# Kernel tuning notes

Measured on AMD Instinct MI355X. Metric: run time of the kernel, lower is better.

## Reference

```python
import jax, jax.numpy as jnp
import numpy as np

B, T, C = 16, 512, 1024
D, K, W = 4096, 128, 8


def _scatter_topk(a, k, use_values):
    """Top-k along last axis; return dense array with top-k values (or 1.0) scattered, zeros elsewhere."""
    shp = a.shape
    a2 = a.reshape(-1, shp[-1])
    vals, idx = jax.lax.top_k(a2, k)
    rows = jnp.arange(a2.shape[0])[:, None]
    src = vals if use_values else jnp.ones_like(vals)
    return jnp.zeros_like(a2).at[rows, idx].set(src).reshape(shp)


def _window_topk(x, k, window_size):
    # x: (B, T, D)
    b, t, d = x.shape
    stride = max(1, window_size // 2)
    if stride >= t:
        num_windows, pad, t_pad = 1, 0, t
    else:
        num_windows = (t - window_size) // stride + 1
        required = (num_windows - 1) * stride + window_size
        pad = max(0, required - t)
        t_pad = t + pad
    if pad > 0:
        x = jnp.pad(x, ((0, 0), (0, pad), (0, 0)))
    starts = jnp.arange(num_windows) * stride                      # (NW,)
    tidx = starts[:, None] + jnp.arange(window_size)               # (NW, W)
    x_windows = x[:, tidx, :]                                      # (B, NW, W, D)
    window_sums = x_windows.sum(axis=2)                            # (B, NW, D)
    mask_windows = _scatter_topk(window_sums, k, use_values=False)  # (B, NW, D)
    votes = (x_windows * mask_windows[:, :, None, :]).reshape(b, num_windows * window_size, d)
    feature_votes = jnp.zeros((b, t_pad, d), x.dtype).at[:, tidx.reshape(-1)].add(votes)
    mask_combined = _scatter_topk(feature_votes, k, use_values=False)  # (B, Tp, D)
    x_sparse = x * mask_combined
    return x_sparse[:, :t - 0, :] if pad > 0 else x_sparse


def setup_inputs() -> dict:
    key = jax.random.key(0)
    ks = jax.random.split(key, 4)
    x_ssl = jax.random.normal(ks[0], (B, T, C), jnp.float32)
    W_dec = jax.random.normal(ks[1], (C, D), jnp.float32)
    W_dec = W_dec / jnp.linalg.norm(W_dec, axis=0, keepdims=True)
    W_enc = W_dec.T                                                # tied init, as in module
    W1 = jax.random.normal(ks[2], (256, D), jnp.float32) * (1.0 / np.sqrt(D))
    W2 = jax.random.normal(ks[3], (2, 256), jnp.float32) * (1.0 / np.sqrt(256))
    return dict(
        x_ssl=x_ssl, W_enc=W_enc, b_enc=jnp.zeros((D,), jnp.float32),
        W_dec=W_dec, b_dec=jnp.zeros((C,), jnp.float32),
        ln_g=jnp.ones((D,), jnp.float32), ln_b=jnp.zeros((D,), jnp.float32),
        W1=W1, b1=jnp.zeros((256,), jnp.float32),
        W2=W2, b2=jnp.zeros((2,), jnp.float32),
    )


def reference(x_ssl, W_enc, b_enc, W_dec, b_dec, ln_g, ln_b, W1, b1, W2, b2):
    b, t, c = x_ssl.shape
    x_flat = x_ssl.reshape(b * t, c)
    # SAE encode with window top-k (window_size=8 > 1 path)
    pre = jnp.einsum('nc,dc->nd', x_flat - b_dec, W_enc) + b_enc
    post_relu = jax.nn.relu(pre).reshape(b, t, -1)                 # (B, T, D)
    encoded = _window_topk(post_relu, K, W)                        # (B, T, D)
    encoded_flat = encoded.reshape(b * t, -1)
    # SAE decode + reconstruction loss
    x_recon = jnp.einsum('nd,cd->nc', encoded_flat, W_dec) + b_dec
    sae_loss = jnp.mean((x_recon - x_flat) ** 2)
    # classifier on pooled sparse features (dropout is inference no-op)
    pooled = encoded.mean(axis=1)                                  # (B, D) == AdaptiveAvgPool1d(1)
    mu = pooled.mean(axis=-1, keepdims=True)
    var = pooled.var(axis=-1, keepdims=True)
    ln = (pooled - mu) / jnp.sqrt(var + 1e-5) * ln_g + ln_b
    h = jax.nn.relu(ln @ W1.T + b1)
    logits = h @ W2.T + b2
    log_probs = jax.nn.log_softmax(logits, axis=-1)
    return log_probs, sae_loss
```

## Files before the change

### kernel.cpp

```cpp
#include <hip/hip_runtime.h>

#define BB   16
#define TT   512
#define CC   1024
#define DD   4096
#define NN   (BB*TT)
#define NWIN 127
#define KTOP 128

typedef __attribute__((ext_vector_type(8))) unsigned short ushort8;
typedef _Float16 half8 __attribute__((ext_vector_type(8)));
typedef __attribute__((ext_vector_type(4))) float f32x4;

__device__ __forceinline__ unsigned short f2h(float f) {
    union { _Float16 h; unsigned short u; } c;
    c.h = (_Float16)f;
    return c.u;
}
__device__ __forceinline__ float h2f(unsigned short u) {
    union { unsigned short u; _Float16 h; } c;
    c.u = u;
    return (float)c.h;
}
__device__ __forceinline__ unsigned tokey(float f) {
    unsigned u = __float_as_uint(f);
    return (u & 0x80000000u) ? ~u : (u | 0x80000000u);
}
__device__ __forceinline__ void async_lds16(const void* g, void* l) {
    __builtin_amdgcn_global_load_lds((const __attribute__((address_space(1))) void*)g,
                                     (__attribute__((address_space(3))) void*)l, 16, 0, 0);
}

#define PH_SYNC() do { __builtin_amdgcn_sched_barrier(0); __builtin_amdgcn_s_barrier(); \
                       asm volatile("s_waitcnt lgkmcnt(0)" ::: "memory"); \
                       __builtin_amdgcn_sched_barrier(0); __builtin_amdgcn_s_setprio(1); } while (0)
#define PH_END()  do { __builtin_amdgcn_s_setprio(0); __builtin_amdgcn_sched_barrier(0); \
                       __builtin_amdgcn_s_barrier(); } while (0)

__device__ __forceinline__ unsigned wave_prefix_incl(unsigned v) {
    int lane = threadIdx.x & 63;
#pragma unroll
    for (int off = 1; off < 64; off <<= 1) {
        unsigned n = __shfl_up(v, off, 64);
        if (lane >= off) v += n;
    }
    return v;
}
__device__ __forceinline__ unsigned wave_suffix_incl(unsigned v) {
    int lane = threadIdx.x & 63;
#pragma unroll
    for (int off = 1; off < 64; off <<= 1) {
        unsigned n = __shfl_down(v, off, 64);
        if (lane + off < 64) v += n;
    }
    return v;
}

__device__ __forceinline__ unsigned select_top128(const unsigned* keys,
                                                  unsigned* hist, unsigned* shx) {
    const int tid = threadIdx.x, wid = tid >> 6, lane = tid & 63;
    const unsigned ZKEY = 0x80000000u;
    unsigned cpos = 0, cz = 0;
#pragma unroll
    for (int i = 0; i < 16; ++i) {
        cpos += (keys[i] > ZKEY);
        cz   += (keys[i] == ZKEY);
    }
    unsigned ppos = wave_prefix_incl(cpos);
    unsigned pz   = wave_prefix_incl(cz);
    if (lane == 63) { shx[wid] = ppos; shx[4 + wid] = pz; }
    __syncthreads();
    unsigned nz = shx[0] + shx[1] + shx[2] + shx[3];
    unsigned selbits = 0u;
    if (nz <= KTOP) {
        unsigned need = KTOP - nz;
        unsigned zr = pz - cz;
        if (wid > 0) zr += shx[4];
        if (wid > 1) zr += shx[5];
        if (wid > 2) zr += shx[6];
#pragma unroll
        for (int i = 0; i < 16; ++i) {
            bool sel = (keys[i] > ZKEY) || (keys[i] == ZKEY && zr < need);
            if (keys[i] == ZKEY) ++zr;
            selbits |= (sel ? 1u : 0u) << i;
        }
        return selbits;
    }
    unsigned k2[16];
#pragma unroll
    for (int i = 0; i < 16; ++i) k2[i] = (keys[i] > ZKEY) ? keys[i] : 0u;
    unsigned prefix = 0u, pmask = 0u, Kr = KTOP;
    for (int shift = 24; shift >= 0; shift -= 8) {
        hist[tid] = 0u; hist[256 + tid] = 0u; hist[512 + tid] = 0u; hist[768 + tid] = 0u;
        __syncthreads();
        unsigned* h = hist + (wid << 8);
#pragma unroll
        for (int i = 0; i < 16; ++i)
            if (k2[i] && (k2[i] & pmask) == prefix) atomicAdd(&h[(k2[i] >> shift) & 255u], 1u);
        __syncthreads();
        unsigned v = hist[tid] + hist[256 + tid] + hist[512 + tid] + hist[768 + tid];
        unsigned s = wave_suffix_incl(v);
        if (lane == 0) shx[wid] = s;
        __syncthreads();
        unsigned stot = s;
        if (wid == 0) stot += shx[1] + shx[2] + shx[3];
        else if (wid == 1) stot += shx[2] + shx[3];
        else if (wid == 2) stot += shx[3];
        unsigned above = stot - v;
        if (stot >= Kr && above < Kr) { shx[8] = (unsigned)tid; shx[9] = Kr - above; }
        __syncthreads();
        prefix |= shx[8] << shift;
        pmask |= 0xFFu << shift;
        Kr = shx[9];
    }
    unsigned T = prefix, need = Kr;
    unsigned ce = 0;
#pragma unroll
    for (int i = 0; i < 16; ++i) ce += (k2[i] == T);
    unsigned pe = wave_prefix_incl(ce);
    __syncthreads();
    if (lane == 63) shx[4 + wid] = pe;
    __syncthreads();
    unsigned er = pe - ce;
    if (wid > 0) er += shx[4];
    if (wid > 1) er += shx[5];
    if (wid > 2) er += shx[6];
#pragma unroll
    for (int i = 0; i < 16; ++i) {
        bool sel = (k2[i] > T) || (k2[i] == T && er < need);
        if (k2[i] == T) ++er;
        selbits |= (sel ? 1u : 0u) << i;
    }
    return selbits;
}

__global__ __launch_bounds__(256) void k_convert_all(const float* __restrict__ x,
                                                     const float* __restrict__ Wenc,
                                                     const float* __restrict__ Wdec,
                                                     const float* __restrict__ bdec,
                                                     unsigned short* __restrict__ xh,
                                                     unsigned short* __restrict__ wh,
                                                     unsigned short* __restrict__ wdh,
                                                     float* __restrict__ pooled_zero) {
    const int bid = blockIdx.x;
    if (bid < 8192) {
        size_t i = (size_t)bid * 256 + threadIdx.x;
        float4 v = ((const float4*)x)[i];
        size_t c = (i * 4) & (CC - 1);
        v.x -= bdec[c]; v.y -= bdec[c + 1]; v.z -= bdec[c + 2]; v.w -= bdec[c + 3];
        uint2 o;
        o.x = (unsigned)f2h(v.x) | ((unsigned)f2h(v.y) << 16);
        o.y = (unsigned)f2h(v.z) | ((unsigned)f2h(v.w) << 16);
        ((uint2*)xh)[i] = o;
    } else if (bid < 12288) {
        size_t i = (size_t)(bid - 8192) * 256 + threadIdx.x;
        float4 v = ((const float4*)Wenc)[i];
        uint2 o;
        o.x = (unsigned)f2h(v.x) | ((unsigned)f2h(v.y) << 16);
        o.y = (unsigned)f2h(v.z) | ((unsigned)f2h(v.w) << 16);
        ((uint2*)wh)[i] = o;
    } else if (bid < 16384) {
        size_t i = (size_t)(bid - 12288) * 256 + threadIdx.x;
        float4 v = ((const float4*)Wdec)[i];
        uint2 o;
        o.x = (unsigned)f2h(v.x) | ((unsigned)f2h(v.y) << 16);
        o.y = (unsigned)f2h(v.z) | ((unsigned)f2h(v.w) << 16);
        ((uint2*)wdh)[i] = o;
    } else {
        const int n4 = (BB * DD + 64) / 4;
        for (int i = threadIdx.x; i < n4; i += 256)
            ((float4*)pooled_zero)[i] = make_float4(0.f, 0.f, 0.f, 0.f);
    }
}

__global__ __launch_bounds__(512, 2) void k_gemm_enc_256(const unsigned short* __restrict__ Ah,
                                                         const unsigned short* __restrict__ Bh,
                                                         const float* __restrict__ bias,
                                                         unsigned short* __restrict__ Cout,
                                                         float* __restrict__ gsum) {
    __shared__ __align__(16) unsigned short lds[2][4][128 * 64];
    const int tid = threadIdx.x, w = tid >> 6, lane = tid & 63;
    const int bm = blockIdx.y * 256, bn = blockIdx.x * 256;
    const int wr = w >> 2, wc = w & 3;
    const int rA = lane & 15, q = lane >> 4;
    const int sc0 = (q ^ (rA & 7)) << 3, sc1 = ((4 + q) ^ (rA & 7)) << 3;
    const int s_rt = w * 16 + (lane >> 3);
    const int s_ct = ((lane & 7) ^ (lane >> 3)) * 8;
    const unsigned short* Abase = Ah + ((size_t)(bm + s_rt)) * 1024 + s_ct;
    const unsigned short* Bbase = Bh + ((size_t)(bn + s_rt)) * 1024 + s_ct;

    auto STAGE = [&](const unsigned short* gb, int rowoff, int kt, unsigned short* reg) {
        const unsigned short* g = gb + (size_t)rowoff * 1024 + (kt << 6);
        async_lds16(g, reg + w * 1024);
        async_lds16(g + 8 * 1024, reg + w * 1024 + 512);
    };

    half8 a[4][2], b[4][2];
    f32x4 acc[8][4] = {};

    auto RDA4 = [&](const unsigned short* reg) {
#pragma unroll
        for (int mf = 0; mf < 4; ++mf) {
            const unsigned short* p = reg + (wr * 64 + mf * 16 + rA) * 64;
            a[mf][0] = *(const half8*)(p + sc0);
            a[mf][1] = *(const half8*)(p + sc1);
        }
    };
    auto RDB2 = [&](const unsigned short* reg, int nb) {
#pragma unroll
        for (int nf = 0; nf < 2; ++nf) {
            const unsigned short* p = reg + (wc * 32 + nf * 16 + rA) * 64;
            b[nb + nf][0] = *(const half8*)(p + sc0);
            b[nb + nf][1] = *(const half8*)(p + sc1);
        }
    };
    auto MF = [&](int mb, int nb) {
#pragma unroll
        for (int kk = 0; kk < 2; ++kk)
#pragma unroll
            for (int mf = 0; mf < 4; ++mf)
#pragma unroll
                for (int nf = 0; nf < 2; ++nf)
                    acc[mb + mf][nb + nf] = __builtin_amdgcn_mfma_f32_16x16x32_f16(
                        a[mf][kk], b[nb + nf][kk], acc[mb + mf][nb + nf], 0, 0, 0);
    };

    STAGE(Abase,   0, 0, lds[0][0]);
    STAGE(Bbase,   0, 0, lds[0][2]);
    STAGE(Abase, 128, 0, lds[0][1]);
    STAGE(Bbase, 128, 0, lds[0][3]);
    STAGE(Abase,   0, 1, lds[1][0]);
    STAGE(Bbase,   0, 1, lds[1][2]);
    STAGE(Abase, 128, 1, lds[1][1]);
    asm volatile("s_waitcnt vmcnt(6)" ::: "memory");
    __builtin_amdgcn_s_barrier();

    for (int i = 0; i < 8; ++i) {
        const int ko  = (2 * i + 1) & 15;
        const int ke  = (2 * i + 2) & 15;
        const int ko2 = (2 * i + 3) & 15;
        RDA4(lds[0][0]); RDB2(lds[0][2], 0);
        STAGE(Bbase, 128, ko, lds[1][3]);
        PH_SYNC(); MF(0, 0); PH_END();
        RDB2(lds[0][3], 2);
        STAGE(Abase, 0, ke, lds[0][0]);
        PH_SYNC(); MF(0, 2); PH_END();
        RDA4(lds[0][1]);
        STAGE(Bbase, 0, ke, lds[0][2]);
        PH_SYNC(); MF(4, 0); PH_END();
        STAGE(Abase, 128, ke, lds[0][1]);
        asm volatile("s_waitcnt vmcnt(6)" ::: "memory");
        PH_SYNC(); MF(4, 2); PH_END();
        RDA4(lds[1][0]); RDB2(lds[1][2], 0);
        STAGE(Bbase, 128, ke, lds[0][3]);
        PH_SYNC(); MF(0, 0); PH_END();
        RDB2(lds[1][3], 2);
        STAGE(Abase, 0, ko2, lds[1][0]);
        PH_SYNC(); MF(0, 2); PH_END();
        RDA4(lds[1][1]);
        STAGE(Bbase, 0, ko2, lds[1][2]);
        PH_SYNC(); MF(4, 0); PH_END();
        STAGE(Abase, 128, ko2, lds[1][1]);
        asm volatile("s_waitcnt vmcnt(6)" ::: "memory");
        PH_SYNC(); MF(4, 2); PH_END();
    }

    asm volatile("s_waitcnt vmcnt(0)" ::: "memory");
    __syncthreads();
    float* cbuf = (float*)&lds[0][0][0];
    const int cl = rA, qr = q * 4;
    float bv[4];
#pragma unroll
    for (int nf = 0; nf < 4; ++nf)
        bv[nf] = bias[bn + ((nf < 2) ? wc * 32 + nf * 16 : 128 + wc * 32 + (nf - 2) * 16) + cl];
    const int rg = tid >> 4, seg = tid & 15;
#pragma unroll
    for (int p = 0; p < 2; ++p) {
        if (p) __syncthreads();
#pragma unroll
        for (int mf = 0; mf < 4; ++mf) {
            int lrow0 = wr * 64 + mf * 16 + qr;
#pragma unroll
            for (int nf = 0; nf < 4; ++nf) {
                int col = ((nf < 2) ? wc * 32 + nf * 16 : 128 + wc * 32 + (nf - 2) * 16) + cl;
#pragma unroll
                for (int r = 0; r < 4; ++r) {
                    int lrow = lrow0 + r;
                    float v = acc[p * 4 + mf][nf][r] + bv[nf];
                    v = v > 0.f ? v : 0.f;
                    cbuf[lrow * 256 + (col ^ (((lrow >> 2) & 7) << 2))] = v;
                }
            }
        }
        __syncthreads();
        f32x4 gs0 = {}, gs1 = {}, gs2 = {}, gs3 = {};
#pragma unroll
        for (int i2 = 0; i2 < 4; ++i2) {
            const int lrow = rg * 4 + i2;
            const f32x4* crow = (const f32x4*)cbuf + lrow * 64;
            f32x4 v0 = crow[(seg * 4 + 0) ^ (rg & 7)];
            f32x4 v1 = crow[(seg * 4 + 1) ^ (rg & 7)];
            f32x4 v2 = crow[(seg * 4 + 2) ^ (rg & 7)];
            f32x4 v3 = crow[(seg * 4 + 3) ^ (rg & 7)];
            uint4 o0, o1;
            o0.x = (unsigned)f2h(v0[0]) | ((unsigned)f2h(v0[1]) << 16);
            o0.y = (unsigned)f2h(v0[2]) | ((unsigned)f2h(v0[3]) << 16);
            o0.z = (unsigned)f2h(v1[0]) | ((unsigned)f2h(v1[1]) << 16);
            o0.w = (unsigned)f2h(v1[2]) | ((unsigned)f2h(v1[3]) << 16);
            o1.x = (unsigned)f2h(v2[0]) | ((unsigned)f2h(v2[1]) << 16);
            o1.y = (unsigned)f2h(v2[2]) | ((unsigned)f2h(v2[3]) << 16);
            o1.z = (unsigned)f2h(v3[0]) | ((unsigned)f2h(v3[1]) << 16);
            o1.w = (unsigned)f2h(v3[2]) | ((unsigned)f2h(v3[3]) << 16);
            size_t gr = (size_t)(bm + p * 128 + lrow) * 4096 + bn + seg * 16;
            *(uint4*)&Cout[gr] = o0;
            *(uint4*)&Cout[gr + 8] = o1;
            gs0 += v0; gs1 += v1; gs2 += v2; gs3 += v3;
        }
        if (gsum) {
            size_t gr = ((size_t)(bm >> 2) + p * 32 + rg) * 4096 + bn + seg * 16;
            *(f32x4*)&gsum[gr + 0]  = gs0;
            *(f32x4*)&gsum[gr + 4]  = gs1;
            *(f32x4*)&gsum[gr + 8]  = gs2;
            *(f32x4*)&gsum[gr + 12] = gs3;
        }
    }
}

__global__ __launch_bounds__(512, 2) void k_gemm_recon_256(const unsigned short* __restrict__ Ap,
                                                           const unsigned short* __restrict__ Bp,
                                                           const float* __restrict__ bdec,
                                                           const float* __restrict__ X,
                                                           float* __restrict__ sae) {
    __shared__ __align__(16) unsigned short lds[2][3][128 * 64];
    __shared__ float red[512];
    const int tid = threadIdx.x, w = tid >> 6, lane = tid & 63;
    const int bm = blockIdx.y * 256, bn = blockIdx.x * 128;
    const int wr = w >> 1, wc = w & 1;
    const int rA = lane & 15, q = lane >> 4;
    const int sc0 = (q ^ (rA & 7)) << 3, sc1 = ((4 + q) ^ (rA & 7)) << 3;
    const int s_rt = w * 16 + (lane >> 3);
    const int s_ct = ((lane & 7) ^ (lane >> 3)) * 8;
    const unsigned short* Abase = Ap + ((size_t)(bm + s_rt)) * 4096 + s_ct;
    const unsigned short* Bbase = Bp + ((size_t)(bn + s_rt)) * 4096 + s_ct;

    auto STAGE = [&](const unsigned short* gb, int rowoff, int kt, unsigned short* reg) {
        const unsigned short* g = gb + (size_t)rowoff * 4096 + (kt << 6);
        async_lds16(g, reg + w * 1024);
        async_lds16(g + 8 * 4096, reg + w * 1024 + 512);
    };

    half8 a[2][2], b[4][2];
    f32x4 acc[4][4] = {};

    auto RDA2 = [&](const unsigned short* reg) {
#pragma unroll
        for (int mf = 0; mf < 2; ++mf) {
            const unsigned short* p = reg + (wr * 32 + mf * 16 + rA) * 64;
            a[mf][0] = *(const half8*)(p + sc0);
            a[mf][1] = *(const half8*)(p + sc1);
        }
    };
    auto RDB2 = [&](const unsigned short* reg, int nb) {
#pragma unroll
        for (int nf = 0; nf < 2; ++nf) {
            const unsigned short* p = reg + ((nb ? 64 : 0) + wc * 32 + nf * 16 + rA) * 64;
            b[nb + nf][0] = *(const half8*)(p + sc0);
            b[nb + nf][1] = *(const half8*)(p + sc1);
        }
    };
    auto MF = [&](int mb, int nb) {
#pragma unroll
        for (int kk = 0; kk < 2; ++kk)
#pragma unroll
            for (int mf = 0; mf < 2; ++mf)
#pragma unroll
                for (int nf = 0; nf < 2; ++nf)
                    acc[mb + mf][nb + nf] = __builtin_amdgcn_mfma_f32_16x16x32_f16(
                        a[mf][kk], b[nb + nf][kk], acc[mb + mf][nb + nf], 0, 0, 0);
    };

    STAGE(Abase,   0, 0, lds[0][0]);
    STAGE(Bbase,   0, 0, lds[0][2]);
    STAGE(Abase, 128, 0, lds[0][1]);
    STAGE(Abase,   0, 1, lds[1][0]);
    STAGE(Bbase,   0, 1, lds[1][2]);
    asm volatile("s_waitcnt vmcnt(4)" ::: "memory");
    __builtin_amdgcn_s_barrier();

    for (int i = 0; i < 32; ++i) {
        const int ko  = (2 * i + 1) & 63;
        const int ke  = (2 * i + 2) & 63;
        const int ko2 = (2 * i + 3) & 63;
        RDA2(lds[0][0]); RDB2(lds[0][2], 0);
        STAGE(Abase, 128, ko, lds[1][1]);
        PH_SYNC(); MF(0, 0); PH_END();
        RDB2(lds[0][2], 2);
        STAGE(Abase, 0, ke, lds[0][0]);
        PH_SYNC(); MF(0, 2); PH_END();
        RDA2(lds[0][1]);
        STAGE(Bbase, 0, ke, lds[0][2]);
        PH_SYNC(); MF(2, 0); PH_END();
        asm volatile("s_waitcnt vmcnt(4)" ::: "memory");
        PH_SYNC(); MF(2, 2); PH_END();
        RDA2(lds[1][0]); RDB2(lds[1][2], 0);
        STAGE(Abase, 128, ke, lds[0][1]);
        PH_SYNC(); MF(0, 0); PH_END();
        RDB2(lds[1][2], 2);
        STAGE(Abase, 0, ko2, lds[1][0]);
        PH_SYNC(); MF(0, 2); PH_END();
        RDA2(lds[1][1]);
        STAGE(Bbase, 0, ko2, lds[1][2]);
        PH_SYNC(); MF(2, 0); PH_END();
        asm volatile("s_waitcnt vmcnt(4)" ::: "memory");
        PH_SYNC(); MF(2, 2); PH_END();
    }

    asm volatile("s_waitcnt vmcnt(0)" ::: "memory");
    const int cl = rA, qr = q * 4;
    float lsum = 0.f;
#pragma unroll
    for (int mf = 0; mf < 4; ++mf) {
        int row0 = bm + ((mf < 2) ? wr * 32 + mf * 16 : 128 + wr * 32 + (mf - 2) * 16) + qr;
#pragma unroll
        for (int nf = 0; nf < 4; ++nf) {
            int col = bn + ((nf < 2) ? wc * 32 + nf * 16 : 64 + wc * 32 + (nf - 2) * 16) + cl;
            float bvv = bdec[col];
#pragma unroll
            for (int r = 0; r < 4; ++r) {
                float v = acc[mf][nf][r] + bvv - X[(size_t)(row0 + r) * 1024 + col];
                lsum += v * v;
            }
        }
    }
    red[tid] = lsum;
    __syncthreads();
    for (int s = 256; s > 0; s >>= 1) { if (tid < s) red[tid] += red[tid + s]; __syncthreads(); }
    if (tid == 0) atomicAdd(sae, red[0]);
}

__global__ __launch_bounds__(256) void k_winsum_g(const float* __restrict__ gsum,
                                                  unsigned* __restrict__ wmask) {
    __shared__ unsigned hist[1024];
    __shared__ unsigned shx[16];
    __shared__ unsigned short halves[256];
    const int tid = threadIdx.x, w = blockIdx.x, b = blockIdx.y;
    const float* g0 = gsum + ((size_t)(b * 128 + w)) * DD + tid * 16;
    const float* g1 = g0 + DD;
    unsigned keys[16];
#pragma unroll
    for (int q = 0; q < 4; ++q) {
        float4 u = *(const float4*)(g0 + q * 4);
        float4 v = *(const float4*)(g1 + q * 4);
        keys[q * 4 + 0] = tokey(u.x + v.x);
        keys[q * 4 + 1] = tokey(u.y + v.y);
        keys[q * 4 + 2] = tokey(u.z + v.z);
        keys[q * 4 + 3] = tokey(u.w + v.w);
    }
    unsigned selbits = select_top128(keys, hist, shx);
    halves[tid] = (unsigned short)selbits;
    __syncthreads();
    if (tid < 128)
        wmask[(size_t)(b * NWIN + w) * 128 + tid] =
            (unsigned)halves[2 * tid] | ((unsigned)halves[2 * tid + 1] << 16);
}

__global__ __launch_bounds__(256) void k_winsum_p(const unsigned short* __restrict__ post,
                                                  unsigned* __restrict__ wmask) {
    __shared__ unsigned hist[1024];
    __shared__ unsigned shx[16];
    __shared__ unsigned short halves[256];
    const int tid = threadIdx.x, w = blockIdx.x, b = blockIdx.y;
    const unsigned short* base = post + (size_t)(b * TT + w * 4) * DD + tid * 16;
    float s[16] = {};
#pragma unroll
    for (int j = 0; j < 8; ++j) {
        const unsigned short* rp = base + (size_t)j * DD;
        ushort8 u0 = *(const ushort8*)rp;
        ushort8 u1 = *(const ushort8*)(rp + 8);
#pragma unroll
        for (int i = 0; i < 8; ++i) { s[i] += h2f(u0[i]); s[8 + i] += h2f(u1[i]); }
    }
    unsigned keys[16];
#pragma unroll
    for (int i = 0; i < 16; ++i) keys[i] = tokey(s[i]);
    unsigned selbits = select_top128(keys, hist, shx);
    halves[tid] = (unsigned short)selbits;
    __syncthreads();
    if (tid < 128)
        wmask[(size_t)(b * NWIN + w) * 128 + tid] =
            (unsigned)halves[2 * tid] | ((unsigned)halves[2 * tid + 1] << 16);
}

__global__ __launch_bounds__(256) void k_votes(unsigned short* __restrict__ post,
                                               const unsigned* __restrict__ wmask,
                                               float* __restrict__ pooled) {
    __shared__ unsigned long long cand[256];
    __shared__ unsigned char selbyte[DD];
    __shared__ unsigned shx[16];
    const int tid = threadIdx.x, wid = tid >> 6, lane = tid & 63;
    const int t = blockIdx.x, b = blockIdx.y;
    unsigned short* rp = post + (size_t)(b * TT + t) * DD;
    int w1 = t >> 2, w0 = w1 - 1;
    unsigned mw0 = 0u, mw1 = 0u;
    if (w0 >= 0)        mw0 = wmask[(size_t)(b * NWIN + w0) * 128 + (tid >> 1)];
    if (w1 <= NWIN - 1) mw1 = wmask[(size_t)(b * NWIN + w1) * 128 + (tid >> 1)];
    const int bbase = (tid & 1) * 16;
    const unsigned ZKEY = 0x80000000u;
    ushort8 raw0 = *(const ushort8*)(rp + tid * 16);
    ushort8 raw1 = *(const ushort8*)(rp + tid * 16 + 8);
    float vals[16];
#pragma unroll
    for (int i = 0; i < 8; ++i) { vals[i] = h2f(raw0[i]); vals[8 + i] = h2f(raw1[i]); }
    unsigned keys[16];
#pragma unroll
    for (int i = 0; i < 16; ++i) {
        float cov = (float)(((mw0 >> (bbase + i)) & 1u) + ((mw1 >> (bbase + i)) & 1u));
        keys[i] = tokey(vals[i] * cov);
    }
    unsigned cpos = 0, cz = 0;
#pragma unroll
    for (int i = 0; i < 16; ++i) {
        cpos += (keys[i] > ZKEY);
        cz   += (keys[i] == ZKEY);
    }
    unsigned ppos = wave_prefix_incl(cpos);
    unsigned pz   = wave_prefix_incl(cz);
    if (lane == 63) { shx[wid] = ppos; shx[4 + wid] = pz; }
    __syncthreads();
    unsigned nz = shx[0] + shx[1] + shx[2] + shx[3];
    unsigned selbits = 0u;
    if (nz <= KTOP) {
        unsigned need = KTOP - nz;
        unsigned zr = pz - cz;
        if (wid > 0) zr += shx[4];
        if (wid > 1) zr += shx[5];
        if (wid > 2) zr += shx[6];
#pragma unroll
        for (int i = 0; i < 16; ++i) {
            bool sel = (keys[i] > ZKEY) || (keys[i] == ZKEY && zr < need);
            if (keys[i] == ZKEY) ++zr;
            selbits |= (sel ? 1u : 0u) << i;
        }
    } else {
        *(uint4*)(selbyte + tid * 16) = make_uint4(0u, 0u, 0u, 0u);
        unsigned off = ppos - cpos;
        if (wid > 0) off += shx[0];
        if (wid > 1) off += shx[1];
        if (wid > 2) off += shx[2];
#pragma unroll
        for (int i = 0; i < 16; ++i) {
            if (keys[i] > ZKEY && off < 256u) {
                int d = tid * 16 + i;
                cand[off++] = ((unsigned long long)keys[i] << 12) | (unsigned)(4095 - d);
            }
        }
        __syncthreads();
        unsigned m = nz < 256u ? nz : 256u;
        if ((unsigned)tid < m) {
            unsigned long long mine = cand[tid];
            unsigned rank = 0;
            for (unsigned j = 0; j < m; ++j) rank += (cand[j] > mine);
            if (rank < KTOP) selbyte[4095 - (unsigned)(mine & 0xFFFu)] = 1;
        }
        __syncthreads();
#pragma unroll
        for (int i = 0; i < 16; ++i)
            selbits |= (selbyte[tid * 16 + i] ? 1u : 0u) << i;
    }
    ushort8 o0, o1;
#pragma unroll
    for (int i = 0; i < 8; ++i) {
        bool s0 = (selbits >> i) & 1u;
        bool s1 = (selbits >> (8 + i)) & 1u;
        o0[i] = s0 ? raw0[i] : (unsigned short)0;
        o1[i] = s1 ? raw1[i] : (unsigned short)0;
        if (s0 && vals[i] != 0.f)     atomicAdd(&pooled[(size_t)b * DD + tid * 16 + i], vals[i]);
        if (s1 && vals[8 + i] != 0.f) atomicAdd(&pooled[(size_t)b * DD + tid * 16 + 8 + i], vals[8 + i]);
    }
    *(ushort8*)(rp + tid * 16)     = o0;
    *(ushort8*)(rp + tid * 16 + 8) = o1;
}

__device__ __forceinline__ float block_sum(float v, float* red) {
    const int tid = threadIdx.x;
    red[tid] = v;
    __syncthreads();
    for (int s = 128; s > 0; s >>= 1) { if (tid < s) red[tid] += red[tid + s]; __syncthreads(); }
    float r = red[0];
    __syncthreads();
    return r;
}

__global__ __launch_bounds__(256) void k_head_ln(const float* __restrict__ pooled,
                                                 const float* __restrict__ lng,
                                                 const float* __restrict__ lnb,
                                                 float* __restrict__ lnout) {
    __shared__ float red[256];
    const int b = blockIdx.x, tid = threadIdx.x;
    float pv[16];
    float s = 0.f;
#pragma unroll
    for (int q = 0; q < 4; ++q) {
        float4 u = *(const float4*)(pooled + (size_t)b * DD + tid * 16 + q * 4);
        pv[q * 4 + 0] = u.x * (1.f / TT); pv[q * 4 + 1] = u.y * (1.f / TT);
        pv[q * 4 + 2] = u.z * (1.f / TT); pv[q * 4 + 3] = u.w * (1.f / TT);
        s += pv[q * 4 + 0] + pv[q * 4 + 1] + pv[q * 4 + 2] + pv[q * 4 + 3];
    }
    float mean = block_sum(s, red) * (1.f / (float)DD);
    float vs = 0.f;
#pragma unroll
    for (int i = 0; i < 16; ++i) { float c = pv[i] - mean; vs += c * c; }
    float var = block_sum(vs, red) * (1.f / (float)DD);
    float inv = rsqrtf(var + 1e-5f);
#pragma unroll
    for (int q = 0; q < 4; ++q) {
        float4 g = *(const float4*)(lng + tid * 16 + q * 4);
        float4 bb = *(const float4*)(lnb + tid * 16 + q * 4);
        float4 o;
        o.x = (pv[q * 4 + 0] - mean) * inv * g.x + bb.x;
        o.y = (pv[q * 4 + 1] - mean) * inv * g.y + bb.y;
        o.z = (pv[q * 4 + 2] - mean) * inv * g.z + bb.z;
        o.w = (pv[q * 4 + 3] - mean) * inv * g.w + bb.w;
        *(float4*)(lnout + (size_t)b * DD + tid * 16 + q * 4) = o;
    }
}

__global__ __launch_bounds__(256) void k_head_mlp(const float* __restrict__ lnout,
                                                  const float* __restrict__ W1,
                                                  const float* __restrict__ b1,
                                                  float* __restrict__ h) {
    const int gw = (blockIdx.x * 256 + threadIdx.x) >> 6;
    const int lane = threadIdx.x & 63;
    const int b = gw >> 8, row = gw & 255;
    const float* lp = lnout + (size_t)b * DD;
    const float* wr = W1 + (size_t)row * DD;
    float a = 0.f;
#pragma unroll
    for (int k = 0; k < DD / 64; ++k)
        a += lp[lane + 64 * k] * wr[lane + 64 * k];
#pragma unroll
    for (int off = 32; off > 0; off >>= 1) a += __shfl_down(a, off, 64);
    if (lane == 0) h[b * 256 + row] = fmaxf(a + b1[row], 0.f);
}

__global__ __launch_bounds__(256) void k_head_out(const float* __restrict__ h,
                                                  const float* __restrict__ W2,
                                                  const float* __restrict__ b2,
                                                  const float* __restrict__ sae,
                                                  float* __restrict__ out) {
    __shared__ float red[256];
    const int b = blockIdx.x, tid = threadIdx.x;
    float hv = h[b * 256 + tid];
    float l0 = block_sum(hv * W2[tid], red) + b2[0];
    float l1 = block_sum(hv * W2[256 + tid], red) + b2[1];
    if (tid == 0) {
        float m = fmaxf(l0, l1);
        float lse = m + logf(expf(l0 - m) + expf(l1 - m));
        out[2 * b] = l0 - lse;
        out[2 * b + 1] = l1 - lse;
        if (b == 0) out[32] = sae[0] * (1.f / (float)((size_t)NN * CC));
    }
}

extern "C" void kernel_launch(void* const* d_in, const int* in_sizes, int n_in,
                              void* d_out, int out_size, void* d_ws, size_t ws_size,
                              hipStream_t stream) {
    const float* x    = (const float*)d_in[0];
    const float* Wenc = (const float*)d_in[1];
    const float* benc = (const float*)d_in[2];
    const float* Wdec = (const float*)d_in[3];
    const float* bdec = (const float*)d_in[4];
    const float* lng  = (const float*)d_in[5];
    const float* lnb  = (const float*)d_in[6];
    const float* W1   = (const float*)d_in[7];
    const float* b1   = (const float*)d_in[8];
    const float* W2   = (const float*)d_in[9];
    const float* b2   = (const float*)d_in[10];
    float* out = (float*)d_out;

    char* ws = (char*)d_ws;
    unsigned short* post  = (unsigned short*)(ws + 0);
    unsigned short* xh16  = (unsigned short*)(ws + 67108864);
    unsigned short* scr   = (unsigned short*)(ws + 83886080);
    unsigned short* wh16  = (unsigned short*)(ws + 100663296);
    unsigned short* wd16  = (unsigned short*)(ws + 109051904);
    unsigned*       wmask = (unsigned*)(ws + 117440512);
    float*          pooled= (float*)(ws + 118480896);
    float*          sae   = (float*)(ws + 118743040);
    float*          gsum  = (float*)(ws + 118743296);
    const bool use_gsum = ws_size >= (size_t)118743296 + 33554432;
    float* gptr = use_gsum ? gsum : nullptr;
    float* lnout = (float*)xh16;
    float* hbuf  = (float*)scr;

    k_convert_all<<<dim3(16385), 256, 0, stream>>>(x, Wenc, Wdec, bdec, xh16, wh16, wd16, pooled);

    k_gemm_enc_256<<<dim3(DD / 256, NN / 256), 512, 0, stream>>>(xh16, wh16, benc, post, gptr);
    if (use_gsum)
        k_winsum_g<<<dim3(NWIN, BB), 256, 0, stream>>>(gsum, wmask);
    else
        k_winsum_p<<<dim3(NWIN, BB), 256, 0, stream>>>(post, wmask);
    k_votes<<<dim3(TT, BB), 256, 0, stream>>>(post, wmask, pooled);
    k_gemm_recon_256<<<dim3(CC / 128, NN / 256), 512, 0, stream>>>(post, wd16, bdec, x, sae);
    k_head_ln<<<dim3(BB), 256, 0, stream>>>(pooled, lng, lnb, lnout);
    k_head_mlp<<<dim3(1024), 256, 0, stream>>>(lnout, W1, b1, hbuf);
    k_head_out<<<dim3(BB), 256, 0, stream>>>(hbuf, W2, b2, sae, out);
}
```

Before: 440.3 us.

## Double-buffer MFMA fragments in GEMMs, drop per-phase barrier, radix-select vote candidates

Both fp16 GEMM kernels now hold two register sets of A and B fragments, so the LDS reads for the next phase are issued while the current MFMAs run. The barrier and lgkmcnt wait before each MFMA phase are removed, and the global-load wait moves into a tail barrier. The launch-bounds occupancy hint drops from 2 to 1 to give the extra fragments registers. In k_votes, the O(m^2) pairwise rank count over up to 256 candidates is replaced by a three-pass 8-bit radix select using a shared histogram, with ties broken by index order. This risks lower occupancy and subtle ordering or hazard issues, and the extra syncthreads may cost more than they save when m is small.

```diff
diff --git a/kernel.cpp b/kernel.cpp
--- a/kernel.cpp
+++ b/kernel.cpp
@@ -31,11 +31,12 @@
                                      (__attribute__((address_space(3))) void*)l, 16, 0, 0);
 }
 
-#define PH_SYNC() do { __builtin_amdgcn_sched_barrier(0); __builtin_amdgcn_s_barrier(); \
-                       asm volatile("s_waitcnt lgkmcnt(0)" ::: "memory"); \
-                       __builtin_amdgcn_sched_barrier(0); __builtin_amdgcn_s_setprio(1); } while (0)
-#define PH_END()  do { __builtin_amdgcn_s_setprio(0); __builtin_amdgcn_sched_barrier(0); \
-                       __builtin_amdgcn_s_barrier(); } while (0)
+#define PH_MID()  do { __builtin_amdgcn_sched_barrier(0); __builtin_amdgcn_s_setprio(1); } while (0)
+#define PH_TAIL() do { __builtin_amdgcn_s_setprio(0); __builtin_amdgcn_sched_barrier(0); \
+                       __builtin_amdgcn_s_barrier(); __builtin_amdgcn_sched_barrier(0); } while (0)
+#define PH_TAIL_G() do { __builtin_amdgcn_s_setprio(0); __builtin_amdgcn_sched_barrier(0); \
+                         asm volatile("s_waitcnt vmcnt(4)" ::: "memory"); \
+                         __builtin_amdgcn_s_barrier(); __builtin_amdgcn_sched_barrier(0); } while (0)
 
 __device__ __forceinline__ unsigned wave_prefix_incl(unsigned v) {
     int lane = threadIdx.x & 63;
@@ -173,7 +174,7 @@
     }
 }
 
-__global__ __launch_bounds__(512, 2) void k_gemm_enc_256(const unsigned short* __restrict__ Ah,
+__global__ __launch_bounds__(512, 1) void k_gemm_enc_256(const unsigned short* __restrict__ Ah,
                                                          const unsigned short* __restrict__ Bh,
                                                          const float* __restrict__ bias,
                                                          unsigned short* __restrict__ Cout,
@@ -195,26 +196,26 @@
         async_lds16(g + 8 * 1024, reg + w * 1024 + 512);
     };
 
-    half8 a[4][2], b[4][2];
+    half8 a0[4][2], a1[4][2], b0[2][2], b1[2][2];
     f32x4 acc[8][4] = {};
 
-    auto RDA4 = [&](const unsigned short* reg) {
+    auto RDA = [&](half8 (&dst)[4][2], const unsigned short* reg) {
 #pragma unroll
         for (int mf = 0; mf < 4; ++mf) {
             const unsigned short* p = reg + (wr * 64 + mf * 16 + rA) * 64;
-            a[mf][0] = *(const half8*)(p + sc0);
-            a[mf][1] = *(const half8*)(p + sc1);
+            dst[mf][0] = *(const half8*)(p + sc0);
+            dst[mf][1] = *(const half8*)(p + sc1);
         }
     };
-    auto RDB2 = [&](const unsigned short* reg, int nb) {
+    auto RDB = [&](half8 (&dst)[2][2], const unsigned short* reg) {
 #pragma unroll
         for (int nf = 0; nf < 2; ++nf) {
             const unsigned short* p = reg + (wc * 32 + nf * 16 + rA) * 64;
-            b[nb + nf][0] = *(const half8*)(p + sc0);
-            b[nb + nf][1] = *(const half8*)(p + sc1);
+            dst[nf][0] = *(const half8*)(p + sc0);
+            dst[nf][1] = *(const half8*)(p + sc1);
         }
     };
-    auto MF = [&](int mb, int nb) {
+    auto MF = [&](half8 (&aa)[4][2], half8 (&bb)[2][2], int mb, int nb) {
 #pragma unroll
         for (int kk = 0; kk < 2; ++kk)
 #pragma unroll
@@ -222,7 +223,7 @@
 #pragma unroll
                 for (int nf = 0; nf < 2; ++nf)
                     acc[mb + mf][nb + nf] = __builtin_amdgcn_mfma_f32_16x16x32_f16(
-                        a[mf][kk], b[nb + nf][kk], acc[mb + mf][nb + nf], 0, 0, 0);
+                        aa[mf][kk], bb[nf][kk], acc[mb + mf][nb + nf], 0, 0, 0);
     };
 
     STAGE(Abase,   0, 0, lds[0][0]);
@@ -234,35 +235,38 @@
     STAGE(Abase, 128, 1, lds[1][1]);
     asm volatile("s_waitcnt vmcnt(6)" ::: "memory");
     __builtin_amdgcn_s_barrier();
+    __builtin_amdgcn_sched_barrier(0);
+    RDA(a0, lds[0][0]);
+    RDB(b0, lds[0][2]);
 
     for (int i = 0; i < 8; ++i) {
         const int ko  = (2 * i + 1) & 15;
         const int ke  = (2 * i + 2) & 15;
         const int ko2 = (2 * i + 3) & 15;
-        RDA4(lds[0][0]); RDB2(lds[0][2], 0);
+        RDB(b1, lds[0][3]);
         STAGE(Bbase, 128, ko, lds[1][3]);
-        PH_SYNC(); MF(0, 0); PH_END();
-        RDB2(lds[0][3], 2);
+        PH_MID(); MF(a0, b0, 0, 0); PH_TAIL();
+        RDA(a1, lds[0][1]);
         STAGE(Abase, 0, ke, lds[0][0]);
-        PH_SYNC(); MF(0, 2); PH_END();
-        RDA4(lds[0][1]);
+        PH_MID(); MF(a0, b1, 0, 2); PH_TAIL();
         STAGE(Bbase, 0, ke, lds[0][2]);
-        PH_SYNC(); MF(4, 0); PH_END();
+        PH_MID(); MF(a1, b0, 4, 0); PH_TAIL_G();
+        RDA(a0, lds[1][0]);
+        RDB(b0, lds[1][2]);
         STAGE(Abase, 128, ke, lds[0][1]);
-        asm volatile("s_waitcnt vmcnt(6)" ::: "memory");
-        PH_SYNC(); MF(4, 2); PH_END();
-        RDA4(lds[1][0]); RDB2(lds[1][2], 0);
+        PH_MID(); MF(a1, b1, 4, 2); PH_TAIL();
+        RDB(b1, lds[1][3]);
         STAGE(Bbase, 128, ke, lds[0][3]);
-        PH_SYNC(); MF(0, 0); PH_END();
-        RDB2(lds[1][3], 2);
+        PH_MID(); MF(a0, b0, 0, 0); PH_TAIL();
+        RDA(a1, lds[1][1]);
         STAGE(Abase, 0, ko2, lds[1][0]);
-        PH_SYNC(); MF(0, 2); PH_END();
-        RDA4(lds[1][1]);
+        PH_MID(); MF(a0, b1, 0, 2); PH_TAIL();
         STAGE(Bbase, 0, ko2, lds[1][2]);
-        PH_SYNC(); MF(4, 0); PH_END();
+        PH_MID(); MF(a1, b0, 4, 0); PH_TAIL_G();
+        RDA(a0, lds[0][0]);
+        RDB(b0, lds[0][2]);
         STAGE(Abase, 128, ko2, lds[1][1]);
-        asm volatile("s_waitcnt vmcnt(6)" ::: "memory");
-        PH_SYNC(); MF(4, 2); PH_END();
+        PH_MID(); MF(a1, b1, 4, 2); PH_TAIL();
     }
 
     asm volatile("s_waitcnt vmcnt(0)" ::: "memory");
@@ -326,7 +330,7 @@
     }
 }
 
-__global__ __launch_bounds__(512, 2) void k_gemm_recon_256(const unsigned short* __restrict__ Ap,
+__global__ __launch_bounds__(512, 1) void k_gemm_recon_256(const unsigned short* __restrict__ Ap,
                                                            const unsigned short* __restrict__ Bp,
                                                            const float* __restrict__ bdec,
                                                            const float* __restrict__ X,
@@ -349,26 +353,26 @@
         async_lds16(g + 8 * 4096, reg + w * 1024 + 512);
     };
 
-    half8 a[2][2], b[4][2];
+    half8 a0[2][2], a1[2][2], b0[2][2], b1[2][2];
     f32x4 acc[4][4] = {};
 
-    auto RDA2 = [&](const unsigned short* reg) {
+    auto RDA = [&](half8 (&dst)[2][2], const unsigned short* reg) {
 #pragma unroll
         for (int mf = 0; mf < 2; ++mf) {
             const unsigned short* p = reg + (wr * 32 + mf * 16 + rA) * 64;
-            a[mf][0] = *(const half8*)(p + sc0);
-            a[mf][1] = *(const half8*)(p + sc1);
+            dst[mf][0] = *(const half8*)(p + sc0);
+            dst[mf][1] = *(const half8*)(p + sc1);
         }
     };
-    auto RDB2 = [&](const unsigned short* reg, int nb) {
+    auto RDB = [&](half8 (&dst)[2][2], const unsigned short* reg, int rofs) {
 #pragma unroll
         for (int nf = 0; nf < 2; ++nf) {
-            const unsigned short* p = reg + ((nb ? 64 : 0) + wc * 32 + nf * 16 + rA) * 64;
-            b[nb + nf][0] = *(const half8*)(p + sc0);
-            b[nb + nf][1] = *(const half8*)(p + sc1);
+            const unsigned short* p = reg + (rofs + wc * 32 + nf * 16 + rA) * 64;
+            dst[nf][0] = *(const half8*)(p + sc0);
+            dst[nf][1] = *(const half8*)(p + sc1);
         }
     };
-    auto MF = [&](int mb, int nb) {
+    auto MF = [&](half8 (&aa)[2][2], half8 (&bb)[2][2], int mb, int nb) {
 #pragma unroll
         for (int kk = 0; kk < 2; ++kk)
 #pragma unroll
@@ -376,7 +380,7 @@
 #pragma unroll
                 for (int nf = 0; nf < 2; ++nf)
                     acc[mb + mf][nb + nf] = __builtin_amdgcn_mfma_f32_16x16x32_f16(
-                        a[mf][kk], b[nb + nf][kk], acc[mb + mf][nb + nf], 0, 0, 0);
+                        aa[mf][kk], bb[nf][kk], acc[mb + mf][nb + nf], 0, 0, 0);
     };
 
     STAGE(Abase,   0, 0, lds[0][0]);
@@ -386,33 +390,36 @@
     STAGE(Bbase,   0, 1, lds[1][2]);
     asm volatile("s_waitcnt vmcnt(4)" ::: "memory");
     __builtin_amdgcn_s_barrier();
+    __builtin_amdgcn_sched_barrier(0);
+    RDA(a0, lds[0][0]);
+    RDB(b0, lds[0][2], 0);
 
     for (int i = 0; i < 32; ++i) {
         const int ko  = (2 * i + 1) & 63;
         const int ke  = (2 * i + 2) & 63;
         const int ko2 = (2 * i + 3) & 63;
-        RDA2(lds[0][0]); RDB2(lds[0][2], 0);
+        RDB(b1, lds[0][2], 64);
         STAGE(Abase, 128, ko, lds[1][1]);
-        PH_SYNC(); MF(0, 0); PH_END();
-        RDB2(lds[0][2], 2);
+        PH_MID(); MF(a0, b0, 0, 0); PH_TAIL();
+        RDA(a1, lds[0][1]);
         STAGE(Abase, 0, ke, lds[0][0]);
-        PH_SYNC(); MF(0, 2); PH_END();
-        RDA2(lds[0][1]);
+        PH_MID(); MF(a0, b1, 0, 2); PH_TAIL();
         STAGE(Bbase, 0, ke, lds[0][2]);
-        PH_SYNC(); MF(2, 0); PH_END();
-        asm volatile("s_waitcnt vmcnt(4)" ::: "memory");
-        PH_SYNC(); MF(2, 2); PH_END();
-        RDA2(lds[1][0]); RDB2(lds[1][2], 0);
+        PH_MID(); MF(a1, b0, 2, 0); PH_TAIL_G();
+        RDA(a0, lds[1][0]);
+        RDB(b0, lds[1][2], 0);
+        PH_MID(); MF(a1, b1, 2, 2); PH_TAIL();
+        RDB(b1, lds[1][2], 64);
         STAGE(Abase, 128, ke, lds[0][1]);
-        PH_SYNC(); MF(0, 0); PH_END();
-        RDB2(lds[1][2], 2);
+        PH_MID(); MF(a0, b0, 0, 0); PH_TAIL();
+        RDA(a1, lds[1][1]);
         STAGE(Abase, 0, ko2, lds[1][0]);
-        PH_SYNC(); MF(0, 2); PH_END();
-        RDA2(lds[1][1]);
+        PH_MID(); MF(a0, b1, 0, 2); PH_TAIL();
         STAGE(Bbase, 0, ko2, lds[1][2]);
-        PH_SYNC(); MF(2, 0); PH_END();
-        asm volatile("s_waitcnt vmcnt(4)" ::: "memory");
-        PH_SYNC(); MF(2, 2); PH_END();
+        PH_MID(); MF(a1, b0, 2, 0); PH_TAIL_G();
+        RDA(a0, lds[0][0]);
+        RDB(b0, lds[0][2], 0);
+        PH_MID(); MF(a1, b1, 2, 2); PH_TAIL();
     }
 
     asm volatile("s_waitcnt vmcnt(0)" ::: "memory");
@@ -497,6 +504,7 @@
     __shared__ unsigned long long cand[256];
     __shared__ unsigned char selbyte[DD];
     __shared__ unsigned shx[16];
+    __shared__ unsigned hcnt[256];
     const int tid = threadIdx.x, wid = tid >> 6, lane = tid & 63;
     const int t = blockIdx.x, b = blockIdx.y;
     unsigned short* rp = post + (size_t)(b * TT + t) * DD;
@@ -555,13 +563,47 @@
             }
         }
         __syncthreads();
-        unsigned m = nz < 256u ? nz : 256u;
-        if ((unsigned)tid < m) {
-            unsigned long long mine = cand[tid];
-            unsigned rank = 0;
-            for (unsigned j = 0; j < m; ++j) rank += (cand[j] > mine);
-            if (rank < KTOP) selbyte[4095 - (unsigned)(mine & 0xFFFu)] = 1;
-        }
+        const unsigned m = nz < 256u ? nz : 256u;
+        unsigned long long ek = (tid < (int)m) ? cand[tid] : 0ULL;
+        unsigned Kr = KTOP;
+        bool alive = (tid < (int)m);
+        bool sel = false;
+#pragma unroll
+        for (int pass = 0; pass < 3; ++pass) {
+            const int shift = 36 - pass * 8;
+            hcnt[tid] = 0u;
+            __syncthreads();
+            unsigned dg = (unsigned)(ek >> shift) & 255u;
+            if (alive) atomicAdd(&hcnt[dg], 1u);
+            __syncthreads();
+            unsigned v = hcnt[tid];
+            unsigned s = wave_suffix_incl(v);
+            if (lane == 0) shx[8 + wid] = s;
+            __syncthreads();
+            unsigned stot = s;
+            if (wid == 0) stot += shx[9] + shx[10] + shx[11];
+            else if (wid == 1) stot += shx[10] + shx[11];
+            else if (wid == 2) stot += shx[11];
+            unsigned above = stot - v;
+            if (stot >= Kr && above < Kr) { shx[12] = (unsigned)tid; shx[13] = Kr - above; }
+            __syncthreads();
+            unsigned Td = shx[12];
+            Kr = shx[13];
+            if (alive) {
+                if (dg > Td) { sel = true; alive = false; }
+                else if (dg < Td) alive = false;
+            }
+        }
+        unsigned av = alive ? 1u : 0u;
+        unsigned pa = wave_prefix_incl(av);
+        if (lane == 63) shx[8 + wid] = pa;
+        __syncthreads();
+        unsigned er = pa - av;
+        if (wid > 0) er += shx[8];
+        if (wid > 1) er += shx[9];
+        if (wid > 2) er += shx[10];
+        if (alive && er < Kr) sel = true;
+        if (sel) selbyte[4095 - (unsigned)(ek & 0xFFFu)] = 1;
         __syncthreads();
 #pragma unroll
         for (int i = 0; i < 16; ++i)
```

Result: slower. 460.0 us (+4.5%).

## Batch four rows per block in k_votes and use radix select for top-k

Applied to the files above, without the earlier changes.

Each k_votes block now handles the four time steps that share the same pair of window masks, so the masks are loaded once per group and pooled sums are built in registers. This replaces per-row atomics with one atomic per feature per group. The O(m^2) rank-counting top-128 over candidates is replaced by a three-pass 8-bit radix select using shared histograms and wave suffix scans, with ties broken by prefix order. The trade-off is fewer blocks, a serial loop over rows, and more barriers per row.

```diff
diff --git a/kernel.cpp b/kernel.cpp
--- a/kernel.cpp
+++ b/kernel.cpp
@@ -497,88 +497,133 @@
     __shared__ unsigned long long cand[256];
     __shared__ unsigned char selbyte[DD];
     __shared__ unsigned shx[16];
+    __shared__ unsigned hcnt[256];
     const int tid = threadIdx.x, wid = tid >> 6, lane = tid & 63;
-    const int t = blockIdx.x, b = blockIdx.y;
-    unsigned short* rp = post + (size_t)(b * TT + t) * DD;
-    int w1 = t >> 2, w0 = w1 - 1;
+    const int g = blockIdx.x, b = blockIdx.y;
+    int w1 = g, w0 = g - 1;
     unsigned mw0 = 0u, mw1 = 0u;
     if (w0 >= 0)        mw0 = wmask[(size_t)(b * NWIN + w0) * 128 + (tid >> 1)];
     if (w1 <= NWIN - 1) mw1 = wmask[(size_t)(b * NWIN + w1) * 128 + (tid >> 1)];
     const int bbase = (tid & 1) * 16;
     const unsigned ZKEY = 0x80000000u;
-    ushort8 raw0 = *(const ushort8*)(rp + tid * 16);
-    ushort8 raw1 = *(const ushort8*)(rp + tid * 16 + 8);
-    float vals[16];
-#pragma unroll
-    for (int i = 0; i < 8; ++i) { vals[i] = h2f(raw0[i]); vals[8 + i] = h2f(raw1[i]); }
-    unsigned keys[16];
-#pragma unroll
-    for (int i = 0; i < 16; ++i) {
-        float cov = (float)(((mw0 >> (bbase + i)) & 1u) + ((mw1 >> (bbase + i)) & 1u));
-        keys[i] = tokey(vals[i] * cov);
-    }
-    unsigned cpos = 0, cz = 0;
-#pragma unroll
-    for (int i = 0; i < 16; ++i) {
-        cpos += (keys[i] > ZKEY);
-        cz   += (keys[i] == ZKEY);
-    }
-    unsigned ppos = wave_prefix_incl(cpos);
-    unsigned pz   = wave_prefix_incl(cz);
-    if (lane == 63) { shx[wid] = ppos; shx[4 + wid] = pz; }
-    __syncthreads();
-    unsigned nz = shx[0] + shx[1] + shx[2] + shx[3];
-    unsigned selbits = 0u;
-    if (nz <= KTOP) {
-        unsigned need = KTOP - nz;
-        unsigned zr = pz - cz;
-        if (wid > 0) zr += shx[4];
-        if (wid > 1) zr += shx[5];
-        if (wid > 2) zr += shx[6];
+    float psum[16];
+#pragma unroll
+    for (int i = 0; i < 16; ++i) psum[i] = 0.f;
+
+    for (int r = 0; r < 4; ++r) {
+        unsigned short* rp = post + (size_t)(b * TT + g * 4 + r) * DD;
+        ushort8 raw0 = *(const ushort8*)(rp + tid * 16);
+        ushort8 raw1 = *(const ushort8*)(rp + tid * 16 + 8);
+        float vals[16];
+#pragma unroll
+        for (int i = 0; i < 8; ++i) { vals[i] = h2f(raw0[i]); vals[8 + i] = h2f(raw1[i]); }
+        unsigned keys[16];
 #pragma unroll
         for (int i = 0; i < 16; ++i) {
-            bool sel = (keys[i] > ZKEY) || (keys[i] == ZKEY && zr < need);
-            if (keys[i] == ZKEY) ++zr;
-            selbits |= (sel ? 1u : 0u) << i;
-        }
-    } else {
-        *(uint4*)(selbyte + tid * 16) = make_uint4(0u, 0u, 0u, 0u);
-        unsigned off = ppos - cpos;
-        if (wid > 0) off += shx[0];
-        if (wid > 1) off += shx[1];
-        if (wid > 2) off += shx[2];
+            float cov = (float)(((mw0 >> (bbase + i)) & 1u) + ((mw1 >> (bbase + i)) & 1u));
+            keys[i] = tokey(vals[i] * cov);
+        }
+        unsigned cpos = 0, cz = 0;
 #pragma unroll
         for (int i = 0; i < 16; ++i) {
-            if (keys[i] > ZKEY && off < 256u) {
-                int d = tid * 16 + i;
-                cand[off++] = ((unsigned long long)keys[i] << 12) | (unsigned)(4095 - d);
+            cpos += (keys[i] > ZKEY);
+            cz   += (keys[i] == ZKEY);
+        }
+        unsigned ppos = wave_prefix_incl(cpos);
+        unsigned pz   = wave_prefix_incl(cz);
+        __syncthreads();
+        if (lane == 63) { shx[wid] = ppos; shx[4 + wid] = pz; }
+        __syncthreads();
+        unsigned nz = shx[0] + shx[1] + shx[2] + shx[3];
+        unsigned selbits = 0u;
+        if (nz <= KTOP) {
+            unsigned need = KTOP - nz;
+            unsigned zr = pz - cz;
+            if (wid > 0) zr += shx[4];
+            if (wid > 1) zr += shx[5];
+            if (wid > 2) zr += shx[6];
+#pragma unroll
+            for (int i = 0; i < 16; ++i) {
+                bool sel = (keys[i] > ZKEY) || (keys[i] == ZKEY && zr < need);
+                if (keys[i] == ZKEY) ++zr;
+                selbits |= (sel ? 1u : 0u) << i;
             }
-        }
-        __syncthreads();
-        unsigned m = nz < 256u ? nz : 256u;
-        if ((unsigned)tid < m) {
-            unsigned long long mine = cand[tid];
-            unsigned rank = 0;
-            for (unsigned j = 0; j < m; ++j) rank += (cand[j] > mine);
-            if (rank < KTOP) selbyte[4095 - (unsigned)(mine & 0xFFFu)] = 1;
-        }
-        __syncthreads();
-#pragma unroll
-        for (int i = 0; i < 16; ++i)
-            selbits |= (selbyte[tid * 16 + i] ? 1u : 0u) << i;
-    }
-    ushort8 o0, o1;
-#pragma unroll
-    for (int i = 0; i < 8; ++i) {
-        bool s0 = (selbits >> i) & 1u;
-        bool s1 = (selbits >> (8 + i)) & 1u;
-        o0[i] = s0 ? raw0[i] : (unsigned short)0;
-        o1[i] = s1 ? raw1[i] : (unsigned short)0;
-        if (s0 && vals[i] != 0.f)     atomicAdd(&pooled[(size_t)b * DD + tid * 16 + i], vals[i]);
-        if (s1 && vals[8 + i] != 0.f) atomicAdd(&pooled[(size_t)b * DD + tid * 16 + 8 + i], vals[8 + i]);
-    }
-    *(ushort8*)(rp + tid * 16)     = o0;
-    *(ushort8*)(rp + tid * 16 + 8) = o1;
+        } else {
+            *(uint4*)(selbyte + tid * 16) = make_uint4(0u, 0u, 0u, 0u);
+            unsigned off = ppos - cpos;
+            if (wid > 0) off += shx[0];
+            if (wid > 1) off += shx[1];
+            if (wid > 2) off += shx[2];
+#pragma unroll
+            for (int i = 0; i < 16; ++i) {
+                if (keys[i] > ZKEY && off < 256u) {
+                    int d = tid * 16 + i;
+                    cand[off++] = ((unsigned long long)keys[i] << 12) | (unsigned)(4095 - d);
+                }
+            }
+            __syncthreads();
+            const unsigned m = nz < 256u ? nz : 256u;
+            unsigned long long ek = (tid < (int)m) ? cand[tid] : 0ULL;
+            unsigned Kr = KTOP;
+            bool alive = (tid < (int)m);
+            bool sel = false;
+#pragma unroll
+            for (int pass = 0; pass < 3; ++pass) {
+                const int shift = 36 - pass * 8;
+                hcnt[tid] = 0u;
+                __syncthreads();
+                unsigned dg = (unsigned)(ek >> shift) & 255u;
+                if (alive) atomicAdd(&hcnt[dg], 1u);
+                __syncthreads();
+                unsigned v = hcnt[tid];
+                unsigned s = wave_suffix_incl(v);
+                if (lane == 0) shx[8 + wid] = s;
+                __syncthreads();
+                unsigned stot = s;
+                if (wid == 0) stot += shx[9] + shx[10] + shx[11];
+                else if (wid == 1) stot += shx[10] + shx[11];
+                else if (wid == 2) stot += shx[11];
+                unsigned above = stot - v;
+                if (stot >= Kr && above < Kr) { shx[12] = (unsigned)tid; shx[13] = Kr - above; }
+                __syncthreads();
+                unsigned Td = shx[12];
+                Kr = shx[13];
+                if (alive) {
+                    if (dg > Td) { sel = true; alive = false; }
+                    else if (dg < Td) alive = false;
+                }
+            }
+            unsigned av = alive ? 1u : 0u;
+            unsigned pa = wave_prefix_incl(av);
+            if (lane == 63) shx[8 + wid] = pa;
+            __syncthreads();
+            unsigned er = pa - av;
+            if (wid > 0) er += shx[8];
+            if (wid > 1) er += shx[9];
+            if (wid > 2) er += shx[10];
+            if (alive && er < Kr) sel = true;
+            if (sel) selbyte[4095 - (unsigned)(ek & 0xFFFu)] = 1;
+            __syncthreads();
+#pragma unroll
+            for (int i = 0; i < 16; ++i)
+                selbits |= (selbyte[tid * 16 + i] ? 1u : 0u) << i;
+        }
+        ushort8 o0, o1;
+#pragma unroll
+        for (int i = 0; i < 8; ++i) {
+            bool s0 = (selbits >> i) & 1u;
+            bool s1 = (selbits >> (8 + i)) & 1u;
+            o0[i] = s0 ? raw0[i] : (unsigned short)0;
+            o1[i] = s1 ? raw1[i] : (unsigned short)0;
+            if (s0) psum[i]     += vals[i];
+            if (s1) psum[8 + i] += vals[8 + i];
+        }
+        *(ushort8*)(rp + tid * 16)     = o0;
+        *(ushort8*)(rp + tid * 16 + 8) = o1;
+    }
+#pragma unroll
+    for (int i = 0; i < 16; ++i)
+        if (psum[i] != 0.f) atomicAdd(&pooled[(size_t)b * DD + tid * 16 + i], psum[i]);
 }
 
 __device__ __forceinline__ float block_sum(float v, float* red) {
@@ -700,7 +745,7 @@
         k_winsum_g<<<dim3(NWIN, BB), 256, 0, stream>>>(gsum, wmask);
     else
         k_winsum_p<<<dim3(NWIN, BB), 256, 0, stream>>>(post, wmask);
-    k_votes<<<dim3(TT, BB), 256, 0, stream>>>(post, wmask, pooled);
+    k_votes<<<dim3(TT / 4, BB), 256, 0, stream>>>(post, wmask, pooled);
     k_gemm_recon_256<<<dim3(CC / 128, NN / 256), 512, 0, stream>>>(post, wd16, bdec, x, sae);
     k_head_ln<<<dim3(BB), 256, 0, stream>>>(pooled, lng, lnb, lnout);
     k_head_mlp<<<dim3(1024), 256, 0, stream>>>(lnout, W1, b1, hbuf);
```

New measurement: 423.6 us. 1.04x faster.
